# Kernel tuning notes

Hardware: AMD Instinct MI355X
Metric: run time of the kernel (lower is better)

The kernel has to match this reference:

```python
import jax, jax.numpy as jnp
import numpy as np
from jax import lax

SAMPLE_RATE = 44100.0


def _biquad(x, b0, b1, b2, a1, a2):
    """Direct-form-I biquad over last axis. x: [B,C,S]; coefs: [B,1] (broadcast over C).
    y[n] = b0*x[n] + b1*x[n-1] + b2*x[n-2] - a1*y[n-1] - a2*y[n-2], zero initial state
    (identical to torchaudio.functional.biquad)."""

    def step(carry, xn):  # xn: [B,C]
        x1, x2, y1, y2 = carry
        y = b0 * xn + b1 * x1 + b2 * x2 - a1 * y1 - a2 * y2
        return (xn, x1, y, y1), y

    xs = jnp.moveaxis(x, -1, 0)  # [S,B,C]
    z = jnp.zeros_like(x[..., 0])
    _, ys = lax.scan(step, (z, z, z, z), xs)
    return jnp.moveaxis(ys, 0, -1)  # [B,C,S]


def _peaking_coeffs(freq, gain, q):
    """RBJ peaking EQ coefficients, normalized by a0. Inputs: [B] -> outputs [B,1]."""
    w0 = 2.0 * jnp.pi * freq / SAMPLE_RATE
    alpha = jnp.sin(w0) / (2.0 * q)
    A = jnp.power(10.0, gain / 40.0)
    cosw0 = jnp.cos(w0)
    b0 = 1.0 + alpha * A
    b1 = -2.0 * cosw0
    b2 = 1.0 - alpha * A
    a0 = 1.0 + alpha / A
    a1 = -2.0 * cosw0
    a2 = 1.0 - alpha / A
    coefs = (b0 / a0, b1 / a0, b2 / a0, a1 / a0, a2 / a0)
    return tuple(c[:, None] for c in coefs)  # broadcast over channel dim


def setup_inputs() -> dict:
    key = jax.random.key(0)
    k1, k2, k3, k4 = jax.random.split(key, 4)
    B, C, S, NB = 32, 2, 262144, 10
    audio = jax.random.normal(k1, (B, C, S), dtype=jnp.float32)
    center_freqs = jax.random.uniform(k2, (B, NB), dtype=jnp.float32, minval=100.0, maxval=10000.0)
    gains = jax.random.uniform(k3, (B, NB), dtype=jnp.float32, minval=-12.0, maxval=12.0)
    q_factors = jax.random.uniform(k4, (B, NB), dtype=jnp.float32, minval=0.5, maxval=4.0)
    return {"audio": audio, "center_freqs": center_freqs, "gains": gains, "q_factors": q_factors}


def reference(audio, center_freqs, gains, q_factors):
    num_bands = center_freqs.shape[1]
    out = audio
    for band in range(num_bands):  # fixed small cascade of structurally distinct filters
        b0, b1, b2, a1, a2 = _peaking_coeffs(center_freqs[:, band], gains[:, band], q_factors[:, band])
        out = _biquad(out, b0, b1, b2, a1, a2)
    return out
```

## Files before the change

### kernel.cpp

```cpp
#include <hip/hip_runtime.h>


#define B_   32
#define C_   2
#define S_   262144
#define NB   10
#define SEQ  64

#define F_LCH   64
#define F_PCH   4096
#define F_G     8
#define F_GRP   512
#define F_NPOW  11
#define NT      4

#define F_OFF_POW 1600
#define F_OFF_T   142400
#define F_OFF_G   5385280
#define F_OFF_SB  6040640
#define F_TOT     6696000


__global__ __launch_bounds__(256) void setup_kernel(
    const float* __restrict__ freqs, const float* __restrict__ gains,
    const float* __restrict__ qs, float* __restrict__ coef,
    float* __restrict__ powers) {
  __shared__ float bufA[400], bufB[400];
  __shared__ float cfs[NB * 5];
  const int b = blockIdx.x, tid = threadIdx.x;
  for (int e = tid; e < 400; e += 256) bufA[e] = 0.0f;
  if (tid < NB) {
    int idx = b * NB + tid;
    float f = freqs[idx], g = gains[idx], Q = qs[idx];
    float w0 = 6.28318530717958648f * f / 44100.0f;
    float sw = sinf(w0), cw = cosf(w0);
    float alpha = sw / (2.0f * Q);
    float A = expf(g * 0.05756462732485114f);
    float aA = alpha * A, adA = alpha / A;
    float inv = 1.0f / (1.0f + adA);
    float c0 = (1.0f + aA) * inv;
    float c1 = -2.0f * cw * inv;
    float c2 = (1.0f - aA) * inv;
    float c3 = 2.0f * cw * inv;
    float c4 = -(1.0f - adA) * inv;
    cfs[tid*5+0] = c0; cfs[tid*5+1] = c1; cfs[tid*5+2] = c2;
    cfs[tid*5+3] = c3; cfs[tid*5+4] = c4;
    float* o = coef + idx * 5;
    o[0] = c0; o[1] = c1; o[2] = c2; o[3] = c3; o[4] = c4;
  }
  __syncthreads();
  if (tid < 20) {
    int c = tid;
    float rp = 0.0f;
    for (int k = 0; k < NB; k++) {
      float b0 = cfs[k*5+0], b1 = cfs[k*5+1], b2 = cfs[k*5+2];
      float na1 = cfs[k*5+3], na2 = cfs[k*5+4];
      float val = (k > 0) ? b0 * rp : 0.0f;
      if (k > 0) {
        if (c == 2*k-2) val += b1;
        if (c == 2*k-1) val += b2;
      }
      if (c == 2*k)   val += na1;
      if (c == 2*k+1) val += na2;
      bufA[2*k*20 + c] = val;
      rp = val;
      if (c == 2*k) bufA[(2*k+1)*20 + c] = 1.0f;
    }
  }
  __syncthreads();
  float* cur = bufA;
  float* nxt = bufB;
  float* pw = powers + (size_t)b * F_NPOW * 400;
  for (int j = 1; j <= 17; j++) {
    for (int e = tid; e < 400; e += 256) {
      int r = e / 20, c = e % 20;
      float acc = 0.0f;
      #pragma unroll
      for (int k = 0; k < 20; k++) acc = fmaf(cur[r*20+k], cur[k*20+c], acc);
      nxt[e] = acc;
    }
    __syncthreads();
    { float* t_ = cur; cur = nxt; nxt = t_; }
    int slot = -1;
    if (j == 6) slot = 0;
    else if (j == 8) slot = 1;
    else if (j == 9) slot = 2;
    else if (j >= 10) slot = j - 7;
    if (slot >= 0) for (int e = tid; e < 400; e += 256) pw[slot*400 + e] = cur[e];
  }
}

__device__ __forceinline__ void stage_tile(const float* xseq, float4* dst,
                                           int tile, int lane) {
  const float4* gx = (const float4*)(xseq + (size_t)tile * 4096);
  #pragma unroll
  for (int it = 0; it < 16; it++) {
    const int f = it * 64 + lane;
    const int c = f >> 4;
    const int gi = (c << 4) | ((f & 15) ^ (c & 15));
    __builtin_amdgcn_global_load_lds(
        (const __attribute__((address_space(1))) void*)(gx + gi),
        (__attribute__((address_space(3))) void*)(dst + it * 64),
        16, 0, 0);
  }
}

template <bool WRITE_OUT>
__device__ __forceinline__ void prefetch_es(
    const float* xseq, const float* tst, int seq, int tile, int lane,
    float2& pe, float4 (&pst)[5]) {
  if (tile > 0) {
    const float2* ep = (const float2*)(xseq + (size_t)tile * 4096) - 1;
    pe = *ep;
  } else {
    pe = make_float2(0.f, 0.f);
  }
  if constexpr (WRITE_OUT) {
    const int chunk = tile * F_LCH + lane;
    const int cm1 = chunk > 0 ? chunk - 1 : 0;
    const int jj = cm1 & 7, gg = cm1 >> 3;
    const float4* sv = (const float4*)tst +
                       (((size_t)seq * 8 + jj) * 5) * 512 + gg;
    #pragma unroll
    for (int i = 0; i < 5; i++) pst[i] = sv[i * 512];
  }
}

template <bool WRITE_OUT>
__global__ __launch_bounds__(64) void pass_v4(
    const float* __restrict__ x, const float* __restrict__ coef,
    const float* __restrict__ tst, float* __restrict__ tout,
    float* __restrict__ out) {
  __shared__ float4 lds4[2048];
  const int seq = blockIdx.y;
  const int b = seq >> 1;
  const int lane = threadIdx.x;
  const int tile0 = blockIdx.x * NT;
  const float* cf = coef + b * NB * 5;
  float b0[NB], b1[NB], b2[NB], na1[NB], na2[NB];
  #pragma unroll
  for (int k = 0; k < NB; k++) {
    b0[k] = cf[k*5+0]; b1[k] = cf[k*5+1]; b2[k] = cf[k*5+2];
    na1[k] = cf[k*5+3]; na2[k] = cf[k*5+4];
  }
  const float* xseq = x + (size_t)seq * S_;

  float2 peC = make_float2(0.f, 0.f), peN = make_float2(0.f, 0.f);
  float4 pstC[5] = {}, pstN[5] = {};

  stage_tile(xseq, lds4, tile0, lane);
  prefetch_es<WRITE_OUT>(xseq, tst, seq, tile0, lane, peC, pstC);

  #pragma unroll 1
  for (int t = 0; t < NT; t++) {
    const int tile = tile0 + t;
    float4* lbuf = lds4 + ((t & 1) << 10);
    asm volatile("s_waitcnt vmcnt(0) lgkmcnt(0)" ::: "memory");
    __builtin_amdgcn_sched_barrier(0);
    if (t + 1 < NT) {
      stage_tile(xseq, lds4 + (((t + 1) & 1) << 10), tile + 1, lane);
      prefetch_es<WRITE_OUT>(xseq, tst, seq, tile + 1, lane, peN, pstN);
    }
    const int chunk = tile * F_LCH + lane;
    float x1, x2;
    if (lane == 0) {
      x1 = peC.y; x2 = peC.x;
    } else {
      float4 pv = lbuf[(lane-1)*16 + (15 ^ ((lane-1) & 15))];
      x2 = pv.z; x1 = pv.w;
    }
    float p[NB], q_[NB];
    if (WRITE_OUT) {
      const bool z = (chunk == 0);
      #pragma unroll
      for (int i = 0; i < 5; i++) {
        float4 a = pstC[i];
        p[2*i]   = z ? 0.f : a.x;  q_[2*i]   = z ? 0.f : a.y;
        p[2*i+1] = z ? 0.f : a.z;  q_[2*i+1] = z ? 0.f : a.w;
      }
    } else {
      #pragma unroll
      for (int k = 0; k < NB; k++) { p[k] = 0.0f; q_[k] = 0.0f; }
    }
    #pragma unroll 2
    for (int qq = 0; qq < 16; qq++) {
      const int slot = lane*16 + (qq ^ (lane & 15));
      float4 xv = lbuf[slot];
      float xin[4] = {xv.x, xv.y, xv.z, xv.w};
      float o[4];
      #pragma unroll
      for (int j = 0; j < 4; j++) {
        float u = xin[j], u1 = x1, u2 = x2;
        x2 = x1; x1 = xin[j];
        #pragma unroll
        for (int k = 0; k < NB; k++) {
          float v = fmaf(b0[k], u,
                    fmaf(b1[k], u1,
                    fmaf(b2[k], u2,
                    fmaf(na1[k], p[k], na2[k] * q_[k]))));
          u1 = p[k]; u2 = q_[k];
          q_[k] = p[k]; p[k] = v;
          u = v;
        }
        o[j] = u;
      }
      if (WRITE_OUT) lbuf[slot] = make_float4(o[0], o[1], o[2], o[3]);
    }
    if (WRITE_OUT) {
      asm volatile("" ::: "memory");
      float4* gy = (float4*)(out + (size_t)seq * S_ + (size_t)tile * 4096);
      #pragma unroll 4
      for (int it = 0; it < 16; it++) {
        int f = it * 64 + lane;
        int c = f >> 4, q = f & 15;
        gy[f] = lbuf[c*16 + (q ^ (c & 15))];
      }
    } else {
      const int jj = chunk & 7, gg = chunk >> 3;
      float4* td = (float4*)tout + (((size_t)seq * 8 + jj) * 5) * 512 + gg;
      td[0]    = make_float4(p[0], q_[0], p[1], q_[1]);
      td[512]  = make_float4(p[2], q_[2], p[3], q_[3]);
      td[1024] = make_float4(p[4], q_[4], p[5], q_[5]);
      td[1536] = make_float4(p[6], q_[6], p[7], q_[7]);
      td[2048] = make_float4(p[8], q_[8], p[9], q_[9]);
    }
    peC = peN;
    #pragma unroll
    for (int i = 0; i < 5; i++) pstC[i] = pstN[i];
  }
}

__device__ __forceinline__ void matvec_acc(const float* M,
                                           const float* v, float* acc) {
  #pragma unroll
  for (int c = 0; c < 20; c++) {
    float vc = v[c];
    const float4* col = (const float4*)&M[c*20];
    float4 c0 = col[0], c1 = col[1], c2 = col[2], c3 = col[3], c4 = col[4];
    acc[0]  = fmaf(c0.x, vc, acc[0]);  acc[1]  = fmaf(c0.y, vc, acc[1]);
    acc[2]  = fmaf(c0.z, vc, acc[2]);  acc[3]  = fmaf(c0.w, vc, acc[3]);
    acc[4]  = fmaf(c1.x, vc, acc[4]);  acc[5]  = fmaf(c1.y, vc, acc[5]);
    acc[6]  = fmaf(c1.z, vc, acc[6]);  acc[7]  = fmaf(c1.w, vc, acc[7]);
    acc[8]  = fmaf(c2.x, vc, acc[8]);  acc[9]  = fmaf(c2.y, vc, acc[9]);
    acc[10] = fmaf(c2.z, vc, acc[10]); acc[11] = fmaf(c2.w, vc, acc[11]);
    acc[12] = fmaf(c3.x, vc, acc[12]); acc[13] = fmaf(c3.y, vc, acc[13]);
    acc[14] = fmaf(c3.z, vc, acc[14]); acc[15] = fmaf(c3.w, vc, acc[15]);
    acc[16] = fmaf(c4.x, vc, acc[16]); acc[17] = fmaf(c4.y, vc, acc[17]);
    acc[18] = fmaf(c4.z, vc, acc[18]); acc[19] = fmaf(c4.w, vc, acc[19]);
  }
}

template <bool WRITE_BACK>
__global__ __launch_bounds__(128) void scan_horner(
    float* __restrict__ t, const float* __restrict__ powers,
    float* __restrict__ gbuf, const float* __restrict__ sbuf) {
  __shared__ float Msh[400];
  const int seq = blockIdx.y, b = seq >> 1;
  const int g = blockIdx.x * 128 + threadIdx.x;
  const float* pw0 = powers + (size_t)b * F_NPOW * 400;
  for (int e = threadIdx.x; e < 400; e += 128) {
    int r = e / 20, c = e % 20;
    Msh[c*20 + r] = pw0[e];
  }
  __syncthreads();
  float s[20];
  if (WRITE_BACK) {
    const float4* sv = (const float4*)(sbuf + ((size_t)seq * F_GRP + g) * 20);
    #pragma unroll
    for (int i = 0; i < 5; i++) {
      float4 a = sv[i];
      s[4*i] = a.x; s[4*i+1] = a.y; s[4*i+2] = a.z; s[4*i+3] = a.w;
    }
  } else {
    #pragma unroll
    for (int r = 0; r < 20; r++) s[r] = 0.0f;
  }
  const float4* tb = (const float4*)t + (size_t)seq * 40 * 512 + g;
  float4* tw = (float4*)t + (size_t)seq * 40 * 512 + g;
  float4 nx[5];
  #pragma unroll
  for (int i = 0; i < 5; i++) nx[i] = tb[i * 512];
  #pragma unroll 1
  for (int j = 0; j < F_G; j++) {
    float ns[20];
    #pragma unroll
    for (int i = 0; i < 5; i++) {
      float4 a = nx[i];
      ns[4*i] = a.x; ns[4*i+1] = a.y; ns[4*i+2] = a.z; ns[4*i+3] = a.w;
    }
    if (j < F_G - 1) {
      const float4* np = tb + (size_t)(j + 1) * 5 * 512;
      #pragma unroll
      for (int i = 0; i < 5; i++) nx[i] = np[i * 512];
    }
    matvec_acc(Msh, s, ns);
    #pragma unroll
    for (int r = 0; r < 20; r++) s[r] = ns[r];
    if (WRITE_BACK) {
      float4* wp = tw + (size_t)j * 5 * 512;
      wp[0]    = make_float4(s[0],  s[1],  s[2],  s[3]);
      wp[512]  = make_float4(s[4],  s[5],  s[6],  s[7]);
      wp[1024] = make_float4(s[8],  s[9],  s[10], s[11]);
      wp[1536] = make_float4(s[12], s[13], s[14], s[15]);
      wp[2048] = make_float4(s[16], s[17], s[18], s[19]);
    }
  }
  if (!WRITE_BACK) {
    float4* gw = (float4*)(gbuf + ((size_t)seq * F_GRP + g) * 20);
    #pragma unroll
    for (int i = 0; i < 5; i++)
      gw[i] = make_float4(s[4*i], s[4*i+1], s[4*i+2], s[4*i+3]);
  }
}

__global__ __launch_bounds__(512) void scan_ks(
    const float* __restrict__ gbuf, const float* __restrict__ powers,
    float* __restrict__ sbuf) {
  __shared__ float h[F_GRP * 20];
  __shared__ float Ksh[400];
  const int seq = blockIdx.x, b = seq >> 1, i = threadIdx.x;
  const float* pw = powers + (size_t)b * F_NPOW * 400;
  float own[20];
  {
    const float4* gv = (const float4*)(gbuf + ((size_t)seq * F_GRP + i) * 20);
    #pragma unroll
    for (int k = 0; k < 5; k++) {
      float4 a = gv[k];
      own[4*k] = a.x; own[4*k+1] = a.y; own[4*k+2] = a.z; own[4*k+3] = a.w;
    }
  }
  #pragma unroll
  for (int r = 0; r < 20; r++) h[i*20 + r] = own[r];
  for (int s = 0; s < 9; s++) {
    const int d = 1 << s;
    const float* pwS = pw + (size_t)(2 + s) * 400;
    __syncthreads();
    for (int e = i; e < 400; e += 512) {
      int r = e / 20, c = e % 20;
      Ksh[c*20 + r] = pwS[e];
    }
    float nb[20];
    if (i >= d) {
      const float4* hv = (const float4*)&h[(i - d) * 20];
      #pragma unroll
      for (int k = 0; k < 5; k++) {
        float4 a = hv[k];
        nb[4*k] = a.x; nb[4*k+1] = a.y; nb[4*k+2] = a.z; nb[4*k+3] = a.w;
      }
    }
    __syncthreads();
    if (i >= d) {
      matvec_acc(Ksh, nb, own);
      #pragma unroll
      for (int r = 0; r < 20; r++) h[i*20 + r] = own[r];
    }
  }
  __syncthreads();
  float4* sw = (float4*)(sbuf + ((size_t)seq * F_GRP + i) * 20);
  if (i > 0) {
    const float4* hv = (const float4*)&h[(i - 1) * 20];
    #pragma unroll
    for (int k = 0; k < 5; k++) sw[k] = hv[k];
  } else {
    #pragma unroll
    for (int k = 0; k < 5; k++) sw[k] = make_float4(0.f, 0.f, 0.f, 0.f);
  }
}

extern "C" void kernel_launch(void* const* d_in, const int* in_sizes, int n_in,
                              void* d_out, int out_size, void* d_ws, size_t ws_size,
                              hipStream_t stream) {
  const float* audio = (const float*)d_in[0];
  const float* freqs = (const float*)d_in[1];
  const float* gains = (const float*)d_in[2];
  const float* qs    = (const float*)d_in[3];
  float* out = (float*)d_out;
  float* ws  = (float*)d_ws;
  float* coef   = ws;
  float* powers = ws + F_OFF_POW;
  float* t      = ws + F_OFF_T;
  float* gbuf   = ws + F_OFF_G;
  float* sbuf   = ws + F_OFF_SB;

  hipLaunchKernelGGL(setup_kernel, dim3(B_), dim3(256), 0, stream,
                     freqs, gains, qs, coef, powers);
  hipLaunchKernelGGL((pass_v4<false>), dim3(64 / NT, SEQ), dim3(64), 0, stream,
                     audio, coef, (const float*)nullptr, t, (float*)nullptr);
  hipLaunchKernelGGL((scan_horner<false>), dim3(F_GRP / 128, SEQ), dim3(128),
                     0, stream, t, powers, gbuf, (const float*)nullptr);
  hipLaunchKernelGGL(scan_ks, dim3(SEQ), dim3(512), 0, stream,
                     gbuf, powers, sbuf);
  hipLaunchKernelGGL((scan_horner<true>), dim3(F_GRP / 128, SEQ), dim3(128),
                     0, stream, t, powers, (float*)nullptr, sbuf);
  hipLaunchKernelGGL((pass_v4<true>), dim3(64 / NT, SEQ), dim3(64), 0, stream,
                     audio, coef, t, (float*)nullptr, out);
}
```

Measured before the change: 265.6 us.

## Fuse group-level state scan into filter passes via wavefront shuffle Kogge-Stone

Removes the two scan_horner kernels. Each pass kernel now computes the 8-chunk group prefix of the 20-dim filter state in registers, using three shuffle-based Kogge-Stone steps with the matrix powers M^1, M^2 and M^4 staged in LDS. The setup kernel stores one extra power and writes the low powers transposed, and scan_ks uses shifted power indices. Each block also handles one tile instead of four, which raises block count but drops the double-buffered prefetch, and each lane does extra 20x20 matvec work.

```diff
diff --git a/kernel.cpp b/kernel.cpp
--- a/kernel.cpp
+++ b/kernel.cpp
@@ -11,14 +11,13 @@
 #define F_PCH   4096
 #define F_G     8
 #define F_GRP   512
-#define F_NPOW  11
-#define NT      4
+#define F_NPOW  12
 
 #define F_OFF_POW 1600
-#define F_OFF_T   142400
-#define F_OFF_G   5385280
-#define F_OFF_SB  6040640
-#define F_TOT     6696000
+#define F_OFF_T   155200
+#define F_OFF_G   5398080
+#define F_OFF_SB  6053440
+#define F_TOT     6708800
 
 
 __global__ __launch_bounds__(256) void setup_kernel(
@@ -83,150 +82,18 @@
     { float* t_ = cur; cur = nxt; nxt = t_; }
     int slot = -1;
     if (j == 6) slot = 0;
-    else if (j == 8) slot = 1;
-    else if (j == 9) slot = 2;
-    else if (j >= 10) slot = j - 7;
-    if (slot >= 0) for (int e = tid; e < 400; e += 256) pw[slot*400 + e] = cur[e];
-  }
-}
-
-__device__ __forceinline__ void stage_tile(const float* xseq, float4* dst,
-                                           int tile, int lane) {
-  const float4* gx = (const float4*)(xseq + (size_t)tile * 4096);
-  #pragma unroll
-  for (int it = 0; it < 16; it++) {
-    const int f = it * 64 + lane;
-    const int c = f >> 4;
-    const int gi = (c << 4) | ((f & 15) ^ (c & 15));
-    __builtin_amdgcn_global_load_lds(
-        (const __attribute__((address_space(1))) void*)(gx + gi),
-        (__attribute__((address_space(3))) void*)(dst + it * 64),
-        16, 0, 0);
-  }
-}
-
-template <bool WRITE_OUT>
-__device__ __forceinline__ void prefetch_es(
-    const float* xseq, const float* tst, int seq, int tile, int lane,
-    float2& pe, float4 (&pst)[5]) {
-  if (tile > 0) {
-    const float2* ep = (const float2*)(xseq + (size_t)tile * 4096) - 1;
-    pe = *ep;
-  } else {
-    pe = make_float2(0.f, 0.f);
-  }
-  if constexpr (WRITE_OUT) {
-    const int chunk = tile * F_LCH + lane;
-    const int cm1 = chunk > 0 ? chunk - 1 : 0;
-    const int jj = cm1 & 7, gg = cm1 >> 3;
-    const float4* sv = (const float4*)tst +
-                       (((size_t)seq * 8 + jj) * 5) * 512 + gg;
-    #pragma unroll
-    for (int i = 0; i < 5; i++) pst[i] = sv[i * 512];
-  }
-}
-
-template <bool WRITE_OUT>
-__global__ __launch_bounds__(64) void pass_v4(
-    const float* __restrict__ x, const float* __restrict__ coef,
-    const float* __restrict__ tst, float* __restrict__ tout,
-    float* __restrict__ out) {
-  __shared__ float4 lds4[2048];
-  const int seq = blockIdx.y;
-  const int b = seq >> 1;
-  const int lane = threadIdx.x;
-  const int tile0 = blockIdx.x * NT;
-  const float* cf = coef + b * NB * 5;
-  float b0[NB], b1[NB], b2[NB], na1[NB], na2[NB];
-  #pragma unroll
-  for (int k = 0; k < NB; k++) {
-    b0[k] = cf[k*5+0]; b1[k] = cf[k*5+1]; b2[k] = cf[k*5+2];
-    na1[k] = cf[k*5+3]; na2[k] = cf[k*5+4];
-  }
-  const float* xseq = x + (size_t)seq * S_;
-
-  float2 peC = make_float2(0.f, 0.f), peN = make_float2(0.f, 0.f);
-  float4 pstC[5] = {}, pstN[5] = {};
-
-  stage_tile(xseq, lds4, tile0, lane);
-  prefetch_es<WRITE_OUT>(xseq, tst, seq, tile0, lane, peC, pstC);
-
-  #pragma unroll 1
-  for (int t = 0; t < NT; t++) {
-    const int tile = tile0 + t;
-    float4* lbuf = lds4 + ((t & 1) << 10);
-    asm volatile("s_waitcnt vmcnt(0) lgkmcnt(0)" ::: "memory");
-    __builtin_amdgcn_sched_barrier(0);
-    if (t + 1 < NT) {
-      stage_tile(xseq, lds4 + (((t + 1) & 1) << 10), tile + 1, lane);
-      prefetch_es<WRITE_OUT>(xseq, tst, seq, tile + 1, lane, peN, pstN);
-    }
-    const int chunk = tile * F_LCH + lane;
-    float x1, x2;
-    if (lane == 0) {
-      x1 = peC.y; x2 = peC.x;
-    } else {
-      float4 pv = lbuf[(lane-1)*16 + (15 ^ ((lane-1) & 15))];
-      x2 = pv.z; x1 = pv.w;
-    }
-    float p[NB], q_[NB];
-    if (WRITE_OUT) {
-      const bool z = (chunk == 0);
-      #pragma unroll
-      for (int i = 0; i < 5; i++) {
-        float4 a = pstC[i];
-        p[2*i]   = z ? 0.f : a.x;  q_[2*i]   = z ? 0.f : a.y;
-        p[2*i+1] = z ? 0.f : a.z;  q_[2*i+1] = z ? 0.f : a.w;
+    else if (j == 7) slot = 1;
+    else if (j == 8) slot = 2;
+    else if (j >= 9) slot = j - 6;
+    if (slot >= 0) {
+      if (slot < 3) {
+        for (int e = tid; e < 400; e += 256)
+          pw[slot*400 + (e % 20) * 20 + e / 20] = cur[e];
+      } else {
+        for (int e = tid; e < 400; e += 256)
+          pw[slot*400 + e] = cur[e];
       }
-    } else {
-      #pragma unroll
-      for (int k = 0; k < NB; k++) { p[k] = 0.0f; q_[k] = 0.0f; }
-    }
-    #pragma unroll 2
-    for (int qq = 0; qq < 16; qq++) {
-      const int slot = lane*16 + (qq ^ (lane & 15));
-      float4 xv = lbuf[slot];
-      float xin[4] = {xv.x, xv.y, xv.z, xv.w};
-      float o[4];
-      #pragma unroll
-      for (int j = 0; j < 4; j++) {
-        float u = xin[j], u1 = x1, u2 = x2;
-        x2 = x1; x1 = xin[j];
-        #pragma unroll
-        for (int k = 0; k < NB; k++) {
-          float v = fmaf(b0[k], u,
-                    fmaf(b1[k], u1,
-                    fmaf(b2[k], u2,
-                    fmaf(na1[k], p[k], na2[k] * q_[k]))));
-          u1 = p[k]; u2 = q_[k];
-          q_[k] = p[k]; p[k] = v;
-          u = v;
-        }
-        o[j] = u;
-      }
-      if (WRITE_OUT) lbuf[slot] = make_float4(o[0], o[1], o[2], o[3]);
-    }
-    if (WRITE_OUT) {
-      asm volatile("" ::: "memory");
-      float4* gy = (float4*)(out + (size_t)seq * S_ + (size_t)tile * 4096);
-      #pragma unroll 4
-      for (int it = 0; it < 16; it++) {
-        int f = it * 64 + lane;
-        int c = f >> 4, q = f & 15;
-        gy[f] = lbuf[c*16 + (q ^ (c & 15))];
-      }
-    } else {
-      const int jj = chunk & 7, gg = chunk >> 3;
-      float4* td = (float4*)tout + (((size_t)seq * 8 + jj) * 5) * 512 + gg;
-      td[0]    = make_float4(p[0], q_[0], p[1], q_[1]);
-      td[512]  = make_float4(p[2], q_[2], p[3], q_[3]);
-      td[1024] = make_float4(p[4], q_[4], p[5], q_[5]);
-      td[1536] = make_float4(p[6], q_[6], p[7], q_[7]);
-      td[2048] = make_float4(p[8], q_[8], p[9], q_[9]);
-    }
-    peC = peN;
-    #pragma unroll
-    for (int i = 0; i < 5; i++) pstC[i] = pstN[i];
+    }
   }
 }
 
@@ -250,66 +117,169 @@
   }
 }
 
-template <bool WRITE_BACK>
-__global__ __launch_bounds__(128) void scan_horner(
-    float* __restrict__ t, const float* __restrict__ powers,
-    float* __restrict__ gbuf, const float* __restrict__ sbuf) {
-  __shared__ float Msh[400];
-  const int seq = blockIdx.y, b = seq >> 1;
-  const int g = blockIdx.x * 128 + threadIdx.x;
-  const float* pw0 = powers + (size_t)b * F_NPOW * 400;
-  for (int e = threadIdx.x; e < 400; e += 128) {
-    int r = e / 20, c = e % 20;
-    Msh[c*20 + r] = pw0[e];
-  }
-  __syncthreads();
-  float s[20];
-  if (WRITE_BACK) {
-    const float4* sv = (const float4*)(sbuf + ((size_t)seq * F_GRP + g) * 20);
+__device__ __forceinline__ void ks_step(float* s, const float* M, int d,
+                                        int lanem) {
+  float t[20];
+  #pragma unroll
+  for (int r = 0; r < 20; r++) t[r] = __shfl_up(s[r], d, 64);
+  float ns[20];
+  #pragma unroll
+  for (int r = 0; r < 20; r++) ns[r] = s[r];
+  matvec_acc(M, t, ns);
+  const bool c = (lanem >= d);
+  #pragma unroll
+  for (int r = 0; r < 20; r++) s[r] = c ? ns[r] : s[r];
+}
+
+template <bool WRITE_OUT>
+__global__ __launch_bounds__(64) void pass_v5(
+    const float* __restrict__ x, const float* __restrict__ coef,
+    const float* __restrict__ powers, float* __restrict__ t,
+    float* __restrict__ aux,
+    float* __restrict__ out) {
+  __shared__ float4 smem[1024 + 320];
+  const int seq = blockIdx.y;
+  const int b = seq >> 1;
+  const int lane = threadIdx.x;
+  const int lanem = lane & 7;
+  const int tile = blockIdx.x;
+  const int chunk = tile * F_LCH + lane;
+  const float* cf = coef + b * NB * 5;
+  float b0[NB], b1[NB], b2[NB], na1[NB], na2[NB];
+  #pragma unroll
+  for (int k = 0; k < NB; k++) {
+    b0[k] = cf[k*5+0]; b1[k] = cf[k*5+1]; b2[k] = cf[k*5+2];
+    na1[k] = cf[k*5+3]; na2[k] = cf[k*5+4];
+  }
+  const float* xseq = x + (size_t)seq * S_;
+
+  const float4* pwv4 = (const float4*)(powers + (size_t)b * F_NPOW * 400);
+  #pragma unroll
+  for (int it = 0; it < 5; it++) {
+    __builtin_amdgcn_global_load_lds(
+        (const __attribute__((address_space(1))) void*)(pwv4 + it * 64 + lane),
+        (__attribute__((address_space(3))) void*)(smem + 1024 + it * 64),
+        16, 0, 0);
+  }
+  {
+    const float4* gx = (const float4*)(xseq + (size_t)tile * 4096);
+    #pragma unroll
+    for (int it = 0; it < 16; it++) {
+      const int f = it * 64 + lane;
+      const int c = f >> 4;
+      const int gi = (c << 4) | ((f & 15) ^ (c & 15));
+      __builtin_amdgcn_global_load_lds(
+          (const __attribute__((address_space(1))) void*)(gx + gi),
+          (__attribute__((address_space(3))) void*)(smem + it * 64),
+          16, 0, 0);
+    }
+  }
+  float2 pe = make_float2(0.f, 0.f);
+  if (tile > 0) {
+    const float2* ep = (const float2*)(xseq + (size_t)tile * 4096) - 1;
+    pe = *ep;
+  }
+  float4 tw4[5], sb4[5];
+  if constexpr (WRITE_OUT) {
+    const int cm1 = (chunk > 0) ? chunk - 1 : 0;
+    const int jj = cm1 & 7, gg = cm1 >> 3;
+    const float4* tvp = (const float4*)t + ((size_t)seq * 8 + jj) * 5 * 512 + gg;
+    #pragma unroll
+    for (int i = 0; i < 5; i++) tw4[i] = tvp[i * 512];
+    const int g = chunk >> 3;
+    const float4* sv = (const float4*)(aux + ((size_t)seq * F_GRP + g) * 20);
+    #pragma unroll
+    for (int i = 0; i < 5; i++) sb4[i] = sv[i];
+  }
+
+  asm volatile("s_waitcnt vmcnt(0) lgkmcnt(0)" ::: "memory");
+  __builtin_amdgcn_sched_barrier(0);
+
+  const float* M1 = (const float*)(smem + 1024);
+  const float* M2 = (const float*)(smem + 1024) + 400;
+  const float* M4 = (const float*)(smem + 1024) + 800;
+
+  float p[NB], q_[NB];
+  if constexpr (WRITE_OUT) {
+    float w[20];
+    const bool useS = (lanem == 0);
     #pragma unroll
     for (int i = 0; i < 5; i++) {
-      float4 a = sv[i];
-      s[4*i] = a.x; s[4*i+1] = a.y; s[4*i+2] = a.z; s[4*i+3] = a.w;
-    }
+      float4 a = useS ? sb4[i] : tw4[i];
+      w[4*i] = a.x; w[4*i+1] = a.y; w[4*i+2] = a.z; w[4*i+3] = a.w;
+    }
+    ks_step(w, M1, 1, lanem);
+    ks_step(w, M2, 2, lanem);
+    ks_step(w, M4, 4, lanem);
+    #pragma unroll
+    for (int k = 0; k < NB; k++) { p[k] = w[2*k]; q_[k] = w[2*k+1]; }
   } else {
     #pragma unroll
-    for (int r = 0; r < 20; r++) s[r] = 0.0f;
-  }
-  const float4* tb = (const float4*)t + (size_t)seq * 40 * 512 + g;
-  float4* tw = (float4*)t + (size_t)seq * 40 * 512 + g;
-  float4 nx[5];
-  #pragma unroll
-  for (int i = 0; i < 5; i++) nx[i] = tb[i * 512];
-  #pragma unroll 1
-  for (int j = 0; j < F_G; j++) {
-    float ns[20];
-    #pragma unroll
-    for (int i = 0; i < 5; i++) {
-      float4 a = nx[i];
-      ns[4*i] = a.x; ns[4*i+1] = a.y; ns[4*i+2] = a.z; ns[4*i+3] = a.w;
-    }
-    if (j < F_G - 1) {
-      const float4* np = tb + (size_t)(j + 1) * 5 * 512;
+    for (int k = 0; k < NB; k++) { p[k] = 0.0f; q_[k] = 0.0f; }
+  }
+  float x1, x2;
+  if (lane == 0) {
+    x1 = pe.y; x2 = pe.x;
+  } else {
+    float4 pv = smem[(lane-1)*16 + (15 ^ ((lane-1) & 15))];
+    x2 = pv.z; x1 = pv.w;
+  }
+  #pragma unroll 2
+  for (int qq = 0; qq < 16; qq++) {
+    const int slot = lane*16 + (qq ^ (lane & 15));
+    float4 xv = smem[slot];
+    float xin[4] = {xv.x, xv.y, xv.z, xv.w};
+    float o[4];
+    #pragma unroll
+    for (int j = 0; j < 4; j++) {
+      float u = xin[j], u1 = x1, u2 = x2;
+      x2 = x1; x1 = xin[j];
       #pragma unroll
-      for (int i = 0; i < 5; i++) nx[i] = np[i * 512];
-    }
-    matvec_acc(Msh, s, ns);
-    #pragma unroll
-    for (int r = 0; r < 20; r++) s[r] = ns[r];
-    if (WRITE_BACK) {
-      float4* wp = tw + (size_t)j * 5 * 512;
-      wp[0]    = make_float4(s[0],  s[1],  s[2],  s[3]);
-      wp[512]  = make_float4(s[4],  s[5],  s[6],  s[7]);
-      wp[1024] = make_float4(s[8],  s[9],  s[10], s[11]);
-      wp[1536] = make_float4(s[12], s[13], s[14], s[15]);
-      wp[2048] = make_float4(s[16], s[17], s[18], s[19]);
-    }
-  }
-  if (!WRITE_BACK) {
-    float4* gw = (float4*)(gbuf + ((size_t)seq * F_GRP + g) * 20);
-    #pragma unroll
-    for (int i = 0; i < 5; i++)
-      gw[i] = make_float4(s[4*i], s[4*i+1], s[4*i+2], s[4*i+3]);
+      for (int k = 0; k < NB; k++) {
+        float v = fmaf(b0[k], u,
+                  fmaf(b1[k], u1,
+                  fmaf(b2[k], u2,
+                  fmaf(na1[k], p[k], na2[k] * q_[k]))));
+        u1 = p[k]; u2 = q_[k];
+        q_[k] = p[k]; p[k] = v;
+        u = v;
+      }
+      o[j] = u;
+    }
+    if (WRITE_OUT) smem[slot] = make_float4(o[0], o[1], o[2], o[3]);
+  }
+  if constexpr (WRITE_OUT) {
+    asm volatile("" ::: "memory");
+    float4* gy = (float4*)(out + (size_t)seq * S_ + (size_t)tile * 4096);
+    #pragma unroll 4
+    for (int it = 0; it < 16; it++) {
+      int f = it * 64 + lane;
+      int c = f >> 4, q = f & 15;
+      gy[f] = smem[c*16 + (q ^ (c & 15))];
+    }
+  } else {
+    const int jj = chunk & 7, gg = chunk >> 3;
+    float4* td = (float4*)t + ((size_t)seq * 8 + jj) * 5 * 512 + gg;
+    td[0]    = make_float4(p[0], q_[0], p[1], q_[1]);
+    td[512]  = make_float4(p[2], q_[2], p[3], q_[3]);
+    td[1024] = make_float4(p[4], q_[4], p[5], q_[5]);
+    td[1536] = make_float4(p[6], q_[6], p[7], q_[7]);
+    td[2048] = make_float4(p[8], q_[8], p[9], q_[9]);
+    float s[20];
+    #pragma unroll
+    for (int k = 0; k < NB; k++) { s[2*k] = p[k]; s[2*k+1] = q_[k]; }
+    ks_step(s, M1, 1, lanem);
+    ks_step(s, M2, 2, lanem);
+    ks_step(s, M4, 4, lanem);
+    if (lanem == 7) {
+      const int g = chunk >> 3;
+      float4* gw = (float4*)(aux + ((size_t)seq * F_GRP + g) * 20);
+      gw[0] = make_float4(s[0],  s[1],  s[2],  s[3]);
+      gw[1] = make_float4(s[4],  s[5],  s[6],  s[7]);
+      gw[2] = make_float4(s[8],  s[9],  s[10], s[11]);
+      gw[3] = make_float4(s[12], s[13], s[14], s[15]);
+      gw[4] = make_float4(s[16], s[17], s[18], s[19]);
+    }
   }
 }
 
@@ -333,7 +303,7 @@
   for (int r = 0; r < 20; r++) h[i*20 + r] = own[r];
   for (int s = 0; s < 9; s++) {
     const int d = 1 << s;
-    const float* pwS = pw + (size_t)(2 + s) * 400;
+    const float* pwS = pw + (size_t)(3 + s) * 400;
     __syncthreads();
     for (int e = i; e < 400; e += 512) {
       int r = e / 20, c = e % 20;
@@ -384,14 +354,10 @@
 
   hipLaunchKernelGGL(setup_kernel, dim3(B_), dim3(256), 0, stream,
                      freqs, gains, qs, coef, powers);
-  hipLaunchKernelGGL((pass_v4<false>), dim3(64 / NT, SEQ), dim3(64), 0, stream,
-                     audio, coef, (const float*)nullptr, t, (float*)nullptr);
-  hipLaunchKernelGGL((scan_horner<false>), dim3(F_GRP / 128, SEQ), dim3(128),
-                     0, stream, t, powers, gbuf, (const float*)nullptr);
+  hipLaunchKernelGGL((pass_v5<false>), dim3(F_PCH / F_LCH, SEQ), dim3(64), 0,
+                     stream, audio, coef, powers, t, gbuf, (float*)nullptr);
   hipLaunchKernelGGL(scan_ks, dim3(SEQ), dim3(512), 0, stream,
                      gbuf, powers, sbuf);
-  hipLaunchKernelGGL((scan_horner<true>), dim3(F_GRP / 128, SEQ), dim3(128),
-                     0, stream, t, powers, (float*)nullptr, sbuf);
-  hipLaunchKernelGGL((pass_v4<true>), dim3(64 / NT, SEQ), dim3(64), 0, stream,
-                     audio, coef, t, (float*)nullptr, out);
-}
+  hipLaunchKernelGGL((pass_v5<true>), dim3(F_PCH / F_LCH, SEQ), dim3(64), 0,
+                     stream, audio, coef, powers, t, sbuf, out);
+}
```

Measured after the change: 263.7 us. No clear change (-0.7%).
